# Optimization experiments

Hardware: AMD Instinct MI355X
Metric: run time of the kernel (lower is better)

## Reference

```python
import jax, jax.numpy as jnp
import numpy as np

MODEL_DIM = 512
NUM_HEADS = 8
HEAD_DIM = MODEL_DIM // NUM_HEADS  # 64
NUM_NODE = 1024
CLUSTER = 128
S = 60
EMBED = 0.5


def setup_inputs() -> dict:
    key = jax.random.key(0)
    ks = jax.random.split(key, 16)
    d = MODEL_DIM
    sc = 1.0 / np.sqrt(d)
    inp = {
        "x": jax.random.normal(ks[0], (4, 12, NUM_NODE, d), dtype=jnp.float32),
        "Wq": jax.random.normal(ks[1], (d, d), dtype=jnp.float32) * sc,
        "bq": jnp.zeros((d,), jnp.float32),
        "Wk": jax.random.normal(ks[2], (d, d), dtype=jnp.float32) * sc,
        "bk": jnp.zeros((d,), jnp.float32),
        "Wv": jax.random.normal(ks[3], (d, d), dtype=jnp.float32) * sc,
        "bv": jnp.zeros((d,), jnp.float32),
        "We": jax.random.normal(ks[4], (d, d), dtype=jnp.float32) * sc,
        "be": jnp.zeros((d,), jnp.float32),
        "Wo": jax.random.normal(ks[5], (d, d), dtype=jnp.float32) * sc,
        "bo": jnp.zeros((d,), jnp.float32),
        # adp_pos is initialized to zeros in torch; use small randn for a non-degenerate test
        "adp_pos": jax.random.normal(ks[6], (NUM_NODE, CLUSTER), dtype=jnp.float32) * 0.02,
        "U1": jax.random.normal(ks[7], (HEAD_DIM, S), dtype=jnp.float32) * np.sqrt(2.0 / (HEAD_DIM + S)),
        "U2": jax.random.normal(ks[8], (S, HEAD_DIM), dtype=jnp.float32) * np.sqrt(2.0 / (S + HEAD_DIM)),
    }
    return inp


def _split_heads(t):
    # torch.cat(torch.split(t, head_dim, -1), 0): heads stacked head-major on batch dim
    return jnp.concatenate(jnp.split(t, NUM_HEADS, axis=-1), axis=0)


def _merge_heads(t):
    return jnp.concatenate(jnp.split(t, NUM_HEADS, axis=0), axis=-1)


def _pool_nodes(t):
    # AdaptiveAvgPool2d((CLUSTER, None)) on (B,T,N,D) with N % CLUSTER == 0 -> block mean
    B, T, N, D = t.shape
    return t.reshape(B, T, CLUSTER, N // CLUSTER, D).mean(axis=3)


def reference(x, Wq, bq, Wk, bk, Wv, bv, We, be, Wo, bo, adp_pos, U1, U2):
    q = x @ Wq.T + bq                      # (B,T,N,D)
    k = _pool_nodes(x @ Wk.T + bk)          # (B,T,C,D)
    v = _pool_nodes(x @ Wv.T + bv)          # (B,T,C,D)
    ev = x @ We.T + be                      # (B,T,N,D)

    qh = _split_heads(q)                    # (B*H,T,N,d)
    kh = _split_heads(k)                    # (B*H,T,C,d)
    vh = _split_heads(v)                    # (B*H,T,C,d)
    evh = _split_heads(ev)                  # (B*H,T,N,d)

    # external attention branch: softmax over node dim (-2)
    exa = jax.nn.softmax(evh @ U1, axis=-2)  # (B*H,T,N,S)
    exa_val = (exa @ U2) * EMBED + evh       # (B*H,T,N,d)

    score = jnp.einsum("btnd,btcd->btnc", qh, kh) / np.sqrt(HEAD_DIM)
    score = score + adp_pos[None, None]      # (B*H,T,N,C)
    attn = jax.nn.softmax(score, axis=-1)

    out = attn @ vh + exa_val                # (B*H,T,N,d)
    out = _merge_heads(out)                  # (B,T,N,D)
    return out @ Wo.T + bo
```

## Files before the change

kernel.cpp:

```cpp
#include <hip/hip_runtime.h>


#define LOG2E 1.44269504088896f

typedef __attribute__((ext_vector_type(4))) float f32x4;
typedef __attribute__((ext_vector_type(8))) short bf16x8;

__device__ __forceinline__ unsigned short f2bf(float f) {
    union { float f; unsigned u; } v; v.f = f;
    unsigned r = (v.u + 0x7fffu + ((v.u >> 16) & 1u)) >> 16;
    return (unsigned short)r;
}
__device__ __forceinline__ float bf2f(unsigned short h) {
    union { unsigned u; float f; } v; v.u = ((unsigned)h) << 16;
    return v.f;
}

__global__ void cvt_w(const float* __restrict__ Wq, const float* __restrict__ Wk,
                      const float* __restrict__ Wv, const float* __restrict__ We,
                      const float* __restrict__ Wo, const float* __restrict__ U1,
                      const float* __restrict__ U2,
                      const float* __restrict__ bq, const float* __restrict__ bk,
                      const float* __restrict__ bv, const float* __restrict__ be,
                      unsigned short* __restrict__ Wqe, unsigned short* __restrict__ Wkv,
                      unsigned short* __restrict__ Wob, unsigned short* __restrict__ U1T,
                      unsigned short* __restrict__ U2bT,
                      float* __restrict__ bqe, float* __restrict__ bkv)
{
    int i = blockIdx.x * 256 + threadIdx.x;
    if (i < 524288) {
        int r = i >> 9;
        float v = (r < 512) ? Wq[i] : We[i - 262144];
        Wqe[i] = f2bf(v);
    } else if (i < 1048576) {
        int j = i - 524288; int r = j >> 9;
        float v = (r < 512) ? Wk[j] : Wv[j - 262144];
        Wkv[j] = f2bf(v);
    } else if (i < 1310720) {
        int j = i - 1048576;
        Wob[j] = f2bf(Wo[j]);
    } else if (i < 1314816) {
        int j = i - 1310720; int s = j >> 6, k = j & 63;
        U1T[j] = (s < 60) ? f2bf(U1[k * 60 + s]) : (unsigned short)0;
    } else if (i < 1318912) {
        int j = i - 1314816; int d = j >> 6, s = j & 63;
        U2bT[j] = (s < 60) ? f2bf(U2[s * 64 + d] * 0.5f) : (unsigned short)0;
    } else if (i < 1319936) {
        int j = i - 1318912;
        bqe[j] = (j < 512) ? bq[j] : be[j - 512];
    } else if (i < 1320960) {
        int j = i - 1319936;
        bkv[j] = (j < 512) ? bk[j] : bv[j - 512];
    }
}

__global__ void cvt_x(const float* __restrict__ x, unsigned short* __restrict__ xb)
{
    long i = (long)blockIdx.x * 256 + threadIdx.x;
    float4 v = ((const float4*)x)[i];
    ushort4 o;
    o.x = f2bf(v.x); o.y = f2bf(v.y); o.z = f2bf(v.z); o.w = f2bf(v.w);
    ((ushort4*)xb)[i] = o;
}

__global__ void pool_x(const float* __restrict__ x, unsigned short* __restrict__ xpb)
{
    int i = blockIdx.x * 256 + threadIdx.x;
    int d4 = i & 127;
    int btc = i >> 7;
    int bt = btc >> 7, c = btc & 127;
    const float4* src = (const float4*)x + ((long)(bt * 1024 + c * 8)) * 128 + d4;
    float sx = 0.f, sy = 0.f, sz = 0.f, sw = 0.f;
#pragma unroll
    for (int j = 0; j < 8; j++) {
        float4 v = src[(long)j * 128];
        sx += v.x; sy += v.y; sz += v.z; sw += v.w;
    }
    ushort4 o;
    o.x = f2bf(sx * 0.125f); o.y = f2bf(sy * 0.125f);
    o.z = f2bf(sz * 0.125f); o.w = f2bf(sw * 0.125f);
    ((ushort4*)xpb)[(long)btc * 128 + d4] = o;
}

template <int OUTF32>
__global__ __launch_bounds__(256, 2) void gemm_bt(
    const unsigned short* __restrict__ A, const unsigned short* __restrict__ W,
    const float* __restrict__ bias, void* __restrict__ Cout,
    int M, int N, int K)
{
    __shared__ __attribute__((aligned(16))) unsigned short As[128 * 32];
    __shared__ __attribute__((aligned(16))) unsigned short Bs[128 * 32];
    const int tid = threadIdx.x;
    const int wave = tid >> 6, lane = tid & 63;
    const int quad = lane >> 4, l16 = lane & 15;
    const int m0 = blockIdx.x * 128, n0 = blockIdx.y * 128;
    const int wm = (wave & 1) * 64, wn = (wave >> 1) * 64;

    f32x4 acc[4][4];
#pragma unroll
    for (int i = 0; i < 4; i++)
#pragma unroll
        for (int j = 0; j < 4; j++) acc[i][j] = (f32x4){0.f, 0.f, 0.f, 0.f};

    const int c0 = tid, c1 = tid + 256;
    const int r0 = c0 >> 2, kc0 = (c0 & 3) * 8;
    const int r1 = c1 >> 2, kc1 = (c1 & 3) * 8;

    for (int k0 = 0; k0 < K; k0 += 32) {
        int4 a0 = *(const int4*)(A + (long)(m0 + r0) * K + k0 + kc0);
        int4 a1 = *(const int4*)(A + (long)(m0 + r1) * K + k0 + kc1);
        int4 b0 = *(const int4*)(W + (long)(n0 + r0) * K + k0 + kc0);
        int4 b1 = *(const int4*)(W + (long)(n0 + r1) * K + k0 + kc1);
        __syncthreads();
        *(int4*)&As[c0 * 8] = a0; *(int4*)&As[c1 * 8] = a1;
        *(int4*)&Bs[c0 * 8] = b0; *(int4*)&Bs[c1 * 8] = b1;
        __syncthreads();
        bf16x8 af[4], bfr[4];
#pragma unroll
        for (int t = 0; t < 4; t++)
            af[t] = *(const bf16x8*)&As[(wm + t * 16 + l16) * 32 + quad * 8];
#pragma unroll
        for (int t = 0; t < 4; t++)
            bfr[t] = *(const bf16x8*)&Bs[(wn + t * 16 + l16) * 32 + quad * 8];
#pragma unroll
        for (int tm = 0; tm < 4; tm++)
#pragma unroll
            for (int tn = 0; tn < 4; tn++)
                acc[tm][tn] = __builtin_amdgcn_mfma_f32_16x16x32_bf16(
                    af[tm], bfr[tn], acc[tm][tn], 0, 0, 0);
    }

#pragma unroll
    for (int tm = 0; tm < 4; tm++)
#pragma unroll
        for (int tn = 0; tn < 4; tn++) {
            int cc = n0 + wn + tn * 16 + l16;
            float bv = bias[cc];
#pragma unroll
            for (int r = 0; r < 4; r++) {
                int rr = m0 + wm + tm * 16 + quad * 4 + r;
                float v = acc[tm][tn][r] + bv;
                if (OUTF32) ((float*)Cout)[(long)rr * N + cc] = v;
                else        ((unsigned short*)Cout)[(long)rr * N + cc] = f2bf(v);
            }
        }
}

__global__ __launch_bounds__(256, 2) void ez_kernel(
    const unsigned short* __restrict__ qev, const unsigned short* __restrict__ U1T,
    unsigned short* __restrict__ Z)
{
    __shared__ __attribute__((aligned(16))) unsigned short evs[128 * 72];
    __shared__ __attribute__((aligned(16))) unsigned short u1s[64 * 72];
    int tid = threadIdx.x, bx = blockIdx.x;
    int bt = bx >> 6, h = (bx >> 3) & 7, nb = bx & 7;
    int wave = tid >> 6, lane = tid & 63, quad = lane >> 4, l16 = lane & 15;

#pragma unroll
    for (int i = 0; i < 4; i++) {
        int c = tid + i * 256; int row = c >> 3, kc = (c & 7) * 8;
        *(int4*)&evs[row * 72 + kc] =
            *(const int4*)(qev + ((long)(bt * 1024 + nb * 128 + row)) * 1024 + 512 + h * 64 + kc);
    }
#pragma unroll
    for (int i = 0; i < 2; i++) {
        int c = tid + i * 256; int row = c >> 3, kc = (c & 7) * 8;
        *(int4*)&u1s[row * 72 + kc] = *(const int4*)(U1T + row * 64 + kc);
    }
    __syncthreads();

    f32x4 acc[2][4];
#pragma unroll
    for (int i = 0; i < 2; i++)
#pragma unroll
        for (int t = 0; t < 4; t++) acc[i][t] = (f32x4){0.f, 0.f, 0.f, 0.f};

#pragma unroll
    for (int kt = 0; kt < 2; kt++) {
        bf16x8 a[2], b[4];
#pragma unroll
        for (int i = 0; i < 2; i++)
            a[i] = *(const bf16x8*)&evs[((wave * 2 + i) * 16 + l16) * 72 + kt * 32 + quad * 8];
#pragma unroll
        for (int t = 0; t < 4; t++)
            b[t] = *(const bf16x8*)&u1s[(t * 16 + l16) * 72 + kt * 32 + quad * 8];
#pragma unroll
        for (int i = 0; i < 2; i++)
#pragma unroll
            for (int t = 0; t < 4; t++)
                acc[i][t] = __builtin_amdgcn_mfma_f32_16x16x32_bf16(a[i], b[t], acc[i][t], 0, 0, 0);
    }

    long zb = (long)(bt * 8 + h) * 1024 + nb * 128;
#pragma unroll
    for (int i = 0; i < 2; i++)
#pragma unroll
        for (int t = 0; t < 4; t++) {
            int s = t * 16 + l16;
            if (s < 60) {
#pragma unroll
                for (int r = 0; r < 4; r++) {
                    int rr = (wave * 2 + i) * 16 + quad * 4 + r;
                    Z[(zb + rr) * 60 + s] = f2bf(acc[i][t][r]);
                }
            }
        }
}

__global__ __launch_bounds__(256, 2) void es_kernel(
    const unsigned short* __restrict__ Z, float* __restrict__ mS, float* __restrict__ lSinv)
{
    __shared__ float ms[4][64];
    __shared__ float ls[4][64];
    int tid = threadIdx.x;
    int s = tid & 63, g = tid >> 6;
    long zb = (long)blockIdx.x * 1024 * 60;
    float m = -1e30f, l = 0.f;
    if (s < 60) {
        for (int r = 0; r < 256; r++) {
            float z = bf2f(Z[zb + (long)(g * 256 + r) * 60 + s]);
            float nm = fmaxf(m, z);
            l = l * exp2f((m - nm) * LOG2E) + exp2f((z - nm) * LOG2E);
            m = nm;
        }
    }
    ms[g][s] = m; ls[g][s] = l;
    __syncthreads();
    if (tid < 60) {
        float M = fmaxf(fmaxf(ms[0][tid], ms[1][tid]), fmaxf(ms[2][tid], ms[3][tid]));
        float L = 0.f;
#pragma unroll
        for (int gg = 0; gg < 4; gg++) L += ls[gg][tid] * exp2f((ms[gg][tid] - M) * LOG2E);
        mS[blockIdx.x * 60 + tid] = M;
        lSinv[blockIdx.x * 60 + tid] = 1.0f / L;
    }
}

__global__ __launch_bounds__(256, 2) void att_kernel(
    const unsigned short* __restrict__ qev, const unsigned short* __restrict__ kv,
    const unsigned short* __restrict__ Z, const float* __restrict__ mS,
    const float* __restrict__ lSinv, const float* __restrict__ adp,
    const unsigned short* __restrict__ U2bT, unsigned short* __restrict__ attn_out)
{
    __shared__ __attribute__((aligned(16))) unsigned short khs[128 * 72];
    __shared__ __attribute__((aligned(16))) unsigned short vts[64 * 136];
    __shared__ __attribute__((aligned(16))) unsigned short Ps[128 * 136];
    __shared__ __attribute__((aligned(16))) unsigned short u2s[64 * 72];
    __shared__ float mSs[64];
    __shared__ float lIs[64];

    int tid = threadIdx.x, bx = blockIdx.x;
    int bt = bx >> 6, h = (bx >> 3) & 7, nb = bx & 7;
    int wave = tid >> 6, lane = tid & 63, quad = lane >> 4, l16 = lane & 15;
    int n0 = nb * 128;
    const long kvrow = (long)bt * 128;
    const long qrow0 = (long)bt * 1024 + n0;

#pragma unroll
    for (int i = 0; i < 4; i++) {
        int c = tid + i * 256; int row = c >> 3, kc = (c & 7) * 8;
        *(int4*)&khs[row * 72 + kc] = *(const int4*)(kv + (kvrow + row) * 1024 + h * 64 + kc);
    }
#pragma unroll
    for (int i = 0; i < 4; i++) {
        int c = tid + i * 256; int row = c >> 3, dc = (c & 7) * 8;
        int4 v = *(const int4*)(kv + (kvrow + row) * 1024 + 512 + h * 64 + dc);
        unsigned short* pv = (unsigned short*)&v;
#pragma unroll
        for (int j = 0; j < 8; j++) vts[(dc + j) * 136 + row] = pv[j];
    }
#pragma unroll
    for (int i = 0; i < 2; i++) {
        int c = tid + i * 256; int row = c >> 3, kc = (c & 7) * 8;
        *(int4*)&u2s[row * 72 + kc] = *(const int4*)(U2bT + row * 64 + kc);
    }
    if (tid < 60) {
        mSs[tid] = mS[(bt * 8 + h) * 60 + tid];
        lIs[tid] = lSinv[(bt * 8 + h) * 60 + tid];
    }
    __syncthreads();

    f32x4 sc[2][8];
#pragma unroll
    for (int i = 0; i < 2; i++)
#pragma unroll
        for (int t = 0; t < 8; t++) sc[i][t] = (f32x4){0.f, 0.f, 0.f, 0.f};

#pragma unroll
    for (int kt = 0; kt < 2; kt++) {
        bf16x8 a[2];
#pragma unroll
        for (int i = 0; i < 2; i++)
            a[i] = *(const bf16x8*)(qev + (qrow0 + (wave * 2 + i) * 16 + l16) * 1024
                                    + h * 64 + kt * 32 + quad * 8);
#pragma unroll
        for (int tn = 0; tn < 8; tn++) {
            bf16x8 b = *(const bf16x8*)&khs[(tn * 16 + l16) * 72 + kt * 32 + quad * 8];
#pragma unroll
            for (int i = 0; i < 2; i++)
                sc[i][tn] = __builtin_amdgcn_mfma_f32_16x16x32_bf16(a[i], b, sc[i][tn], 0, 0, 0);
        }
    }

#pragma unroll
    for (int i = 0; i < 2; i++) {
#pragma unroll
        for (int tn = 0; tn < 8; tn++)
#pragma unroll
            for (int r = 0; r < 4; r++) {
                int rr = (wave * 2 + i) * 16 + quad * 4 + r;
                sc[i][tn][r] = sc[i][tn][r] * 0.125f + adp[(n0 + rr) * 128 + tn * 16 + l16];
            }
        float rmax[4], rsum[4];
#pragma unroll
        for (int r = 0; r < 4; r++) {
            float m = sc[i][0][r];
#pragma unroll
            for (int tn = 1; tn < 8; tn++) m = fmaxf(m, sc[i][tn][r]);
#pragma unroll
            for (int d = 1; d < 16; d <<= 1) m = fmaxf(m, __shfl_xor(m, d, 64));
            rmax[r] = m; rsum[r] = 0.f;
        }
#pragma unroll
        for (int tn = 0; tn < 8; tn++)
#pragma unroll
            for (int r = 0; r < 4; r++) {
                float p = exp2f((sc[i][tn][r] - rmax[r]) * LOG2E);
                sc[i][tn][r] = p; rsum[r] += p;
            }
#pragma unroll
        for (int r = 0; r < 4; r++) {
#pragma unroll
            for (int d = 1; d < 16; d <<= 1) rsum[r] += __shfl_xor(rsum[r], d, 64);
            rsum[r] = 1.0f / rsum[r];
        }
#pragma unroll
        for (int tn = 0; tn < 8; tn++)
#pragma unroll
            for (int r = 0; r < 4; r++) {
                int rr = (wave * 2 + i) * 16 + quad * 4 + r;
                Ps[rr * 136 + tn * 16 + l16] = f2bf(sc[i][tn][r] * rsum[r]);
            }
    }
    __syncthreads();

    unsigned short* exs = khs;
    const long zrow0 = (long)(bt * 8 + h) * 1024 + n0;
#pragma unroll
    for (int it = 0; it < 32; it++) {
        int idx = tid + it * 256;
        int rr = idx >> 6, s = idx & 63;
        unsigned short o = 0;
        if (s < 60) {
            float z = bf2f(Z[(zrow0 + rr) * 60 + s]);
            o = f2bf(exp2f((z - mSs[s]) * LOG2E) * lIs[s]);
        }
        exs[rr * 72 + s] = o;
    }
    __syncthreads();

    f32x4 oc[2][4];
#pragma unroll
    for (int i = 0; i < 2; i++)
#pragma unroll
        for (int t = 0; t < 4; t++) oc[i][t] = (f32x4){0.f, 0.f, 0.f, 0.f};

#pragma unroll
    for (int kt = 0; kt < 4; kt++) {
        bf16x8 a[2];
#pragma unroll
        for (int i = 0; i < 2; i++)
            a[i] = *(const bf16x8*)&Ps[((wave * 2 + i) * 16 + l16) * 136 + kt * 32 + quad * 8];
#pragma unroll
        for (int tn = 0; tn < 4; tn++) {
            bf16x8 b = *(const bf16x8*)&vts[(tn * 16 + l16) * 136 + kt * 32 + quad * 8];
#pragma unroll
            for (int i = 0; i < 2; i++)
                oc[i][tn] = __builtin_amdgcn_mfma_f32_16x16x32_bf16(a[i], b, oc[i][tn], 0, 0, 0);
        }
    }
#pragma unroll
    for (int kt = 0; kt < 2; kt++) {
        bf16x8 a[2];
#pragma unroll
        for (int i = 0; i < 2; i++)
            a[i] = *(const bf16x8*)&exs[((wave * 2 + i) * 16 + l16) * 72 + kt * 32 + quad * 8];
#pragma unroll
        for (int tn = 0; tn < 4; tn++) {
            bf16x8 b = *(const bf16x8*)&u2s[(tn * 16 + l16) * 72 + kt * 32 + quad * 8];
#pragma unroll
            for (int i = 0; i < 2; i++)
                oc[i][tn] = __builtin_amdgcn_mfma_f32_16x16x32_bf16(a[i], b, oc[i][tn], 0, 0, 0);
        }
    }

#pragma unroll
    for (int i = 0; i < 2; i++)
#pragma unroll
        for (int tn = 0; tn < 4; tn++)
#pragma unroll
            for (int r = 0; r < 4; r++) {
                int rr = (wave * 2 + i) * 16 + quad * 4 + r;
                int cc = tn * 16 + l16;
                float ev = bf2f(qev[(qrow0 + rr) * 1024 + 512 + h * 64 + cc]);
                attn_out[(qrow0 + rr) * 512 + h * 64 + cc] = f2bf(oc[i][tn][r] + ev);
            }
}

extern "C" void kernel_launch(void* const* d_in, const int* in_sizes, int n_in,
                              void* d_out, int out_size, void* d_ws, size_t ws_size,
                              hipStream_t stream)
{
    const float* x   = (const float*)d_in[0];
    const float* Wq  = (const float*)d_in[1];
    const float* bq  = (const float*)d_in[2];
    const float* Wk  = (const float*)d_in[3];
    const float* bk  = (const float*)d_in[4];
    const float* Wv  = (const float*)d_in[5];
    const float* bv  = (const float*)d_in[6];
    const float* We  = (const float*)d_in[7];
    const float* be  = (const float*)d_in[8];
    const float* Wo  = (const float*)d_in[9];
    const float* bo  = (const float*)d_in[10];
    const float* adp = (const float*)d_in[11];
    const float* U1  = (const float*)d_in[12];
    const float* U2  = (const float*)d_in[13];

    char* ws = (char*)d_ws;
    unsigned short* xb   = (unsigned short*)(ws + 0);
    unsigned short* aout = xb;
    unsigned short* xpb  = (unsigned short*)(ws + 50331648);
    unsigned short* qev  = (unsigned short*)(ws + 56623104);
    unsigned short* kvb  = (unsigned short*)(ws + 157286400);
    unsigned short* Zb   = (unsigned short*)(ws + 169869312);
    unsigned short* Wqe  = (unsigned short*)(ws + 217055232);
    unsigned short* Wkv  = (unsigned short*)(ws + 218103808);
    unsigned short* Wob  = (unsigned short*)(ws + 219152384);
    unsigned short* U1T  = (unsigned short*)(ws + 219676672);
    unsigned short* U2bT = (unsigned short*)(ws + 219684864);
    float*          bqe  = (float*)(ws + 219693056);
    float*          bkv  = (float*)(ws + 219697152);
    float*          mSb  = (float*)(ws + 219701248);
    float*          lIb  = (float*)(ws + 219793408);

    cvt_w<<<5160, 256, 0, stream>>>(Wq, Wk, Wv, We, Wo, U1, U2, bq, bk, bv, be,
                                    Wqe, Wkv, Wob, U1T, U2bT, bqe, bkv);
    cvt_x<<<24576, 256, 0, stream>>>(x, xb);
    pool_x<<<3072, 256, 0, stream>>>(x, xpb);

    gemm_bt<0><<<dim3(384, 8), 256, 0, stream>>>(xb,  Wqe, bqe, (void*)qev, 49152, 1024, 512);
    gemm_bt<0><<<dim3(48, 8),  256, 0, stream>>>(xpb, Wkv, bkv, (void*)kvb,  6144, 1024, 512);

    ez_kernel<<<3072, 256, 0, stream>>>(qev, U1T, Zb);
    es_kernel<<<384, 256, 0, stream>>>(Zb, mSb, lIb);
    att_kernel<<<3072, 256, 0, stream>>>(qev, kvb, Zb, mSb, lIb, adp, U2bT, aout);

    gemm_bt<1><<<dim3(384, 4), 256, 0, stream>>>(aout, Wob, bo, d_out, 49152, 512, 512);
}
```

Baseline: 535.8 us.

## Fuse x conversion with pooling, pre-transpose V in KV GEMM, slim attention LDS

Merges the bf16 conversion of x with the node pooling so x is read once. The KV projection gets a dedicated GEMM whose epilogue writes K contiguously and V already transposed per head. The attention kernel no longer stages K, V, U2 and the external-attention exponentials in shared memory: it reads operands straight from global/L2 and computes the exp values in registers, which cuts LDS use and allows 3 blocks per CU. The cost is more uncoalesced global loads in the MFMA loops, and there are scattered ushort4 stores in the V epilogue.

```diff
diff --git a/kernel.cpp b/kernel.cpp
--- a/kernel.cpp
+++ b/kernel.cpp
@@ -54,32 +54,29 @@
     }
 }
 
-__global__ void cvt_x(const float* __restrict__ x, unsigned short* __restrict__ xb)
-{
-    long i = (long)blockIdx.x * 256 + threadIdx.x;
-    float4 v = ((const float4*)x)[i];
-    ushort4 o;
-    o.x = f2bf(v.x); o.y = f2bf(v.y); o.z = f2bf(v.z); o.w = f2bf(v.w);
-    ((ushort4*)xb)[i] = o;
-}
-
-__global__ void pool_x(const float* __restrict__ x, unsigned short* __restrict__ xpb)
+__global__ void cvt_pool(const float* __restrict__ x, unsigned short* __restrict__ xb,
+                         unsigned short* __restrict__ xpb)
 {
     int i = blockIdx.x * 256 + threadIdx.x;
     int d4 = i & 127;
     int btc = i >> 7;
     int bt = btc >> 7, c = btc & 127;
-    const float4* src = (const float4*)x + ((long)(bt * 1024 + c * 8)) * 128 + d4;
+    long base = ((long)(bt * 1024 + c * 8)) * 128 + d4;
+    const float4* src = (const float4*)x + base;
+    ushort4* dst = (ushort4*)xb + base;
     float sx = 0.f, sy = 0.f, sz = 0.f, sw = 0.f;
 #pragma unroll
     for (int j = 0; j < 8; j++) {
         float4 v = src[(long)j * 128];
         sx += v.x; sy += v.y; sz += v.z; sw += v.w;
-    }
-    ushort4 o;
-    o.x = f2bf(sx * 0.125f); o.y = f2bf(sy * 0.125f);
-    o.z = f2bf(sz * 0.125f); o.w = f2bf(sw * 0.125f);
-    ((ushort4*)xpb)[(long)btc * 128 + d4] = o;
+        ushort4 o;
+        o.x = f2bf(v.x); o.y = f2bf(v.y); o.z = f2bf(v.z); o.w = f2bf(v.w);
+        dst[(long)j * 128] = o;
+    }
+    ushort4 p;
+    p.x = f2bf(sx * 0.125f); p.y = f2bf(sy * 0.125f);
+    p.z = f2bf(sz * 0.125f); p.w = f2bf(sw * 0.125f);
+    ((ushort4*)xpb)[(long)btc * 128 + d4] = p;
 }
 
 template <int OUTF32>
@@ -142,6 +139,79 @@
                 float v = acc[tm][tn][r] + bv;
                 if (OUTF32) ((float*)Cout)[(long)rr * N + cc] = v;
                 else        ((unsigned short*)Cout)[(long)rr * N + cc] = f2bf(v);
+            }
+        }
+}
+
+__global__ __launch_bounds__(256, 2) void g2_kv(
+    const unsigned short* __restrict__ A, const unsigned short* __restrict__ W,
+    const float* __restrict__ bias, unsigned short* __restrict__ kvK,
+    unsigned short* __restrict__ vT)
+{
+    const int M = 6144, N = 1024, K = 512;
+    __shared__ __attribute__((aligned(16))) unsigned short As[128 * 32];
+    __shared__ __attribute__((aligned(16))) unsigned short Bs[128 * 32];
+    const int tid = threadIdx.x;
+    const int wave = tid >> 6, lane = tid & 63;
+    const int quad = lane >> 4, l16 = lane & 15;
+    const int m0 = blockIdx.x * 128, n0 = blockIdx.y * 128;
+    const int wm = (wave & 1) * 64, wn = (wave >> 1) * 64;
+    (void)M;
+
+    f32x4 acc[4][4];
+#pragma unroll
+    for (int i = 0; i < 4; i++)
+#pragma unroll
+        for (int j = 0; j < 4; j++) acc[i][j] = (f32x4){0.f, 0.f, 0.f, 0.f};
+
+    const int c0 = tid, c1 = tid + 256;
+    const int r0 = c0 >> 2, kc0 = (c0 & 3) * 8;
+    const int r1 = c1 >> 2, kc1 = (c1 & 3) * 8;
+
+    for (int k0 = 0; k0 < K; k0 += 32) {
+        int4 a0 = *(const int4*)(A + (long)(m0 + r0) * K + k0 + kc0);
+        int4 a1 = *(const int4*)(A + (long)(m0 + r1) * K + k0 + kc1);
+        int4 b0 = *(const int4*)(W + (long)(n0 + r0) * K + k0 + kc0);
+        int4 b1 = *(const int4*)(W + (long)(n0 + r1) * K + k0 + kc1);
+        __syncthreads();
+        *(int4*)&As[c0 * 8] = a0; *(int4*)&As[c1 * 8] = a1;
+        *(int4*)&Bs[c0 * 8] = b0; *(int4*)&Bs[c1 * 8] = b1;
+        __syncthreads();
+        bf16x8 af[4], bfr[4];
+#pragma unroll
+        for (int t = 0; t < 4; t++)
+            af[t] = *(const bf16x8*)&As[(wm + t * 16 + l16) * 32 + quad * 8];
+#pragma unroll
+        for (int t = 0; t < 4; t++)
+            bfr[t] = *(const bf16x8*)&Bs[(wn + t * 16 + l16) * 32 + quad * 8];
+#pragma unroll
+        for (int tm = 0; tm < 4; tm++)
+#pragma unroll
+            for (int tn = 0; tn < 4; tn++)
+                acc[tm][tn] = __builtin_amdgcn_mfma_f32_16x16x32_bf16(
+                    af[tm], bfr[tn], acc[tm][tn], 0, 0, 0);
+    }
+
+#pragma unroll
+    for (int tm = 0; tm < 4; tm++)
+#pragma unroll
+        for (int tn = 0; tn < 4; tn++) {
+            int cc = n0 + wn + tn * 16 + l16;
+            float bv = bias[cc];
+            int rrb = m0 + wm + tm * 16 + quad * 4;
+            if (cc < 512) {
+#pragma unroll
+                for (int r = 0; r < 4; r++)
+                    kvK[(long)(rrb + r) * 512 + cc] = f2bf(acc[tm][tn][r] + bv);
+            } else {
+                int hh = (cc - 512) >> 6, dd = (cc - 512) & 63;
+                int btv = rrb >> 7, cv = rrb & 127;
+                ushort4 o;
+                o.x = f2bf(acc[tm][tn][0] + bv);
+                o.y = f2bf(acc[tm][tn][1] + bv);
+                o.z = f2bf(acc[tm][tn][2] + bv);
+                o.w = f2bf(acc[tm][tn][3] + bv);
+                *(ushort4*)(vT + ((long)(btv * 8 + hh) * 64 + dd) * 128 + cv) = o;
             }
         }
 }
@@ -236,49 +306,21 @@
     }
 }
 
-__global__ __launch_bounds__(256, 2) void att_kernel(
-    const unsigned short* __restrict__ qev, const unsigned short* __restrict__ kv,
-    const unsigned short* __restrict__ Z, const float* __restrict__ mS,
-    const float* __restrict__ lSinv, const float* __restrict__ adp,
-    const unsigned short* __restrict__ U2bT, unsigned short* __restrict__ attn_out)
-{
-    __shared__ __attribute__((aligned(16))) unsigned short khs[128 * 72];
-    __shared__ __attribute__((aligned(16))) unsigned short vts[64 * 136];
+__global__ __launch_bounds__(256, 3) void att_kernel(
+    const unsigned short* __restrict__ qev, const unsigned short* __restrict__ kvK,
+    const unsigned short* __restrict__ vT, const unsigned short* __restrict__ Z,
+    const float* __restrict__ mS, const float* __restrict__ lI,
+    const float* __restrict__ adp, const unsigned short* __restrict__ U2bT,
+    unsigned short* __restrict__ attn_out)
+{
     __shared__ __attribute__((aligned(16))) unsigned short Ps[128 * 136];
-    __shared__ __attribute__((aligned(16))) unsigned short u2s[64 * 72];
-    __shared__ float mSs[64];
-    __shared__ float lIs[64];
 
     int tid = threadIdx.x, bx = blockIdx.x;
     int bt = bx >> 6, h = (bx >> 3) & 7, nb = bx & 7;
     int wave = tid >> 6, lane = tid & 63, quad = lane >> 4, l16 = lane & 15;
     int n0 = nb * 128;
-    const long kvrow = (long)bt * 128;
+    const int g = bt * 8 + h;
     const long qrow0 = (long)bt * 1024 + n0;
-
-#pragma unroll
-    for (int i = 0; i < 4; i++) {
-        int c = tid + i * 256; int row = c >> 3, kc = (c & 7) * 8;
-        *(int4*)&khs[row * 72 + kc] = *(const int4*)(kv + (kvrow + row) * 1024 + h * 64 + kc);
-    }
-#pragma unroll
-    for (int i = 0; i < 4; i++) {
-        int c = tid + i * 256; int row = c >> 3, dc = (c & 7) * 8;
-        int4 v = *(const int4*)(kv + (kvrow + row) * 1024 + 512 + h * 64 + dc);
-        unsigned short* pv = (unsigned short*)&v;
-#pragma unroll
-        for (int j = 0; j < 8; j++) vts[(dc + j) * 136 + row] = pv[j];
-    }
-#pragma unroll
-    for (int i = 0; i < 2; i++) {
-        int c = tid + i * 256; int row = c >> 3, kc = (c & 7) * 8;
-        *(int4*)&u2s[row * 72 + kc] = *(const int4*)(U2bT + row * 64 + kc);
-    }
-    if (tid < 60) {
-        mSs[tid] = mS[(bt * 8 + h) * 60 + tid];
-        lIs[tid] = lSinv[(bt * 8 + h) * 60 + tid];
-    }
-    __syncthreads();
 
     f32x4 sc[2][8];
 #pragma unroll
@@ -295,7 +337,8 @@
                                     + h * 64 + kt * 32 + quad * 8);
 #pragma unroll
         for (int tn = 0; tn < 8; tn++) {
-            bf16x8 b = *(const bf16x8*)&khs[(tn * 16 + l16) * 72 + kt * 32 + quad * 8];
+            bf16x8 b = *(const bf16x8*)(kvK + (long)(bt * 128 + tn * 16 + l16) * 512
+                                        + h * 64 + kt * 32 + quad * 8);
 #pragma unroll
             for (int i = 0; i < 2; i++)
                 sc[i][tn] = __builtin_amdgcn_mfma_f32_16x16x32_bf16(a[i], b, sc[i][tn], 0, 0, 0);
@@ -342,22 +385,6 @@
                 Ps[rr * 136 + tn * 16 + l16] = f2bf(sc[i][tn][r] * rsum[r]);
             }
     }
-    __syncthreads();
-
-    unsigned short* exs = khs;
-    const long zrow0 = (long)(bt * 8 + h) * 1024 + n0;
-#pragma unroll
-    for (int it = 0; it < 32; it++) {
-        int idx = tid + it * 256;
-        int rr = idx >> 6, s = idx & 63;
-        unsigned short o = 0;
-        if (s < 60) {
-            float z = bf2f(Z[(zrow0 + rr) * 60 + s]);
-            o = f2bf(exp2f((z - mSs[s]) * LOG2E) * lIs[s]);
-        }
-        exs[rr * 72 + s] = o;
-    }
-    __syncthreads();
 
     f32x4 oc[2][4];
 #pragma unroll
@@ -373,24 +400,47 @@
             a[i] = *(const bf16x8*)&Ps[((wave * 2 + i) * 16 + l16) * 136 + kt * 32 + quad * 8];
 #pragma unroll
         for (int tn = 0; tn < 4; tn++) {
-            bf16x8 b = *(const bf16x8*)&vts[(tn * 16 + l16) * 136 + kt * 32 + quad * 8];
+            bf16x8 b = *(const bf16x8*)(vT + ((long)g * 64 + tn * 16 + l16) * 128
+                                        + kt * 32 + quad * 8);
 #pragma unroll
             for (int i = 0; i < 2; i++)
                 oc[i][tn] = __builtin_amdgcn_mfma_f32_16x16x32_bf16(a[i], b, oc[i][tn], 0, 0, 0);
         }
     }
+
 #pragma unroll
     for (int kt = 0; kt < 2; kt++) {
-        bf16x8 a[2];
-#pragma unroll
-        for (int i = 0; i < 2; i++)
-            a[i] = *(const bf16x8*)&exs[((wave * 2 + i) * 16 + l16) * 72 + kt * 32 + quad * 8];
+        int sb = kt * 32 + quad * 8;
+        float4 ma = *(const float4*)(mS + (long)g * 60 + sb);
+        float4 mb2 = *(const float4*)(mS + (long)g * 60 + sb + 4);
+        float4 la = *(const float4*)(lI + (long)g * 60 + sb);
+        float4 lb2 = *(const float4*)(lI + (long)g * 60 + sb + 4);
+        float mv[8] = {ma.x, ma.y, ma.z, ma.w, mb2.x, mb2.y, mb2.z, mb2.w};
+        float lv[8] = {la.x, la.y, la.z, la.w, lb2.x, lb2.y, lb2.z, lb2.w};
+        bf16x8 ea[2];
+#pragma unroll
+        for (int i = 0; i < 2; i++) {
+            int row = (wave * 2 + i) * 16 + l16;
+            const unsigned short* zp = Z + ((long)g * 1024 + n0 + row) * 60 + sb;
+            uint2 z0 = *(const uint2*)zp;
+            uint2 z1 = *(const uint2*)(zp + 4);
+            unsigned zz[4] = {z0.x, z0.y, z1.x, z1.y};
+            unsigned short es_[8];
+#pragma unroll
+            for (int j = 0; j < 8; j++) {
+                unsigned short zh = (unsigned short)((zz[j >> 1] >> ((j & 1) * 16)) & 0xffff);
+                float e = (sb + j < 60)
+                    ? exp2f((bf2f(zh) - mv[j]) * LOG2E) * lv[j] : 0.f;
+                es_[j] = f2bf(e);
+            }
+            ea[i] = *(bf16x8*)es_;
+        }
 #pragma unroll
         for (int tn = 0; tn < 4; tn++) {
-            bf16x8 b = *(const bf16x8*)&u2s[(tn * 16 + l16) * 72 + kt * 32 + quad * 8];
+            bf16x8 b = *(const bf16x8*)(U2bT + (tn * 16 + l16) * 64 + sb);
 #pragma unroll
             for (int i = 0; i < 2; i++)
-                oc[i][tn] = __builtin_amdgcn_mfma_f32_16x16x32_bf16(a[i], b, oc[i][tn], 0, 0, 0);
+                oc[i][tn] = __builtin_amdgcn_mfma_f32_16x16x32_bf16(ea[i], b, oc[i][tn], 0, 0, 0);
         }
     }
 
@@ -431,29 +481,29 @@
     unsigned short* aout = xb;
     unsigned short* xpb  = (unsigned short*)(ws + 50331648);
     unsigned short* qev  = (unsigned short*)(ws + 56623104);
-    unsigned short* kvb  = (unsigned short*)(ws + 157286400);
+    unsigned short* kvK  = (unsigned short*)(ws + 157286400);
+    unsigned short* vT   = (unsigned short*)(ws + 163577856);
     unsigned short* Zb   = (unsigned short*)(ws + 169869312);
     unsigned short* Wqe  = (unsigned short*)(ws + 217055232);
     unsigned short* Wkv  = (unsigned short*)(ws + 218103808);
     unsigned short* Wob  = (unsigned short*)(ws + 219152384);
     unsigned short* U1T  = (unsigned short*)(ws + 219676672);
     unsigned short* U2bT = (unsigned short*)(ws + 219684864);
-    float*          bqe  = (float*)(ws + 219693056);
-    float*          bkv  = (float*)(ws + 219697152);
-    float*          mSb  = (float*)(ws + 219701248);
-    float*          lIb  = (float*)(ws + 219793408);
+    float*          mSb  = (float*)(ws + 219693056);
+    float*          lIb  = (float*)(ws + 219785216);
+    float*          bqe  = (float*)(ws + 219877376);
+    float*          bkv  = (float*)(ws + 219881472);
 
     cvt_w<<<5160, 256, 0, stream>>>(Wq, Wk, Wv, We, Wo, U1, U2, bq, bk, bv, be,
                                     Wqe, Wkv, Wob, U1T, U2bT, bqe, bkv);
-    cvt_x<<<24576, 256, 0, stream>>>(x, xb);
-    pool_x<<<3072, 256, 0, stream>>>(x, xpb);
+    cvt_pool<<<3072, 256, 0, stream>>>(x, xb, xpb);
 
     gemm_bt<0><<<dim3(384, 8), 256, 0, stream>>>(xb,  Wqe, bqe, (void*)qev, 49152, 1024, 512);
-    gemm_bt<0><<<dim3(48, 8),  256, 0, stream>>>(xpb, Wkv, bkv, (void*)kvb,  6144, 1024, 512);
+    g2_kv<<<dim3(48, 8), 256, 0, stream>>>(xpb, Wkv, bkv, kvK, vT);
 
     ez_kernel<<<3072, 256, 0, stream>>>(qev, U1T, Zb);
     es_kernel<<<384, 256, 0, stream>>>(Zb, mSb, lIb);
-    att_kernel<<<3072, 256, 0, stream>>>(qev, kvb, Zb, mSb, lIb, adp, U2bT, aout);
+    att_kernel<<<3072, 256, 0, stream>>>(qev, kvK, vT, Zb, mSb, lIb, adp, U2bT, aout);
 
     gemm_bt<1><<<dim3(384, 4), 256, 0, stream>>>(aout, Wob, bo, d_out, 49152, 512, 512);
 }
```

Result: faster. 477.9 us (-10.8%).
